# Optimization experiments

Measured on AMD Instinct MI355X. Metric: run time of the kernel, lower is better.

Reference implementation:

```python
import jax, jax.numpy as jnp
import numpy as np

B = 16384
A_SCALE = 1.7159
S_SCALE = 2.0 / 3.0
CONNECTIONS = [[0,1,2],[1,2,3],[2,3,4],[3,4,5],[0,4,5],[0,1,5],
               [0,1,2,3],[1,2,3,4],[2,3,4,5],[0,3,4,5],[0,1,4,5],[0,1,2,5],
               [0,1,3,4],[1,2,4,5],[0,2,3,5],[0,1,2,3,4,5]]

def _c3_mask():
    m = np.zeros((16, 6, 1, 1), dtype=np.float32)
    for i, conns in enumerate(CONNECTIONS):
        m[i, conns, 0, 0] = 1.0
    return jnp.asarray(m)

C3_MASK = _c3_mask()

def tanh_act(x):
    return A_SCALE * jnp.tanh(S_SCALE * x)

def conv_valid(x, w):
    # x: (B, Cin, H, W), w: (Cout, Cin, k, k) -> (B, Cout, H-k+1, W-k+1)
    return jax.lax.conv_general_dilated(
        x, w, window_strides=(1, 1), padding='VALID',
        dimension_numbers=('NCHW', 'OIHW', 'NCHW'))

def pool_affine(x, w, b):
    # Faithful to the torch 'efficient' path: reshape(B,C,H/2,W/2,2,2).mean((4,5)).
    # (This is a row-major regrouping, NOT true 2x2 block pooling.)
    bsz, c, h, wd = x.shape
    y = x.reshape(bsz, c, h // 2, wd // 2, 2, 2).mean(axis=(4, 5))
    return w.reshape(1, c, 1, 1) * y + b.reshape(1, c, 1, 1)


def setup_inputs() -> dict:
    key = jax.random.key(0)
    ks = jax.random.split(key, 14)
    inp = {
        'x':     jax.random.normal(ks[0], (B, 1, 32, 32), jnp.float32),
        'w1':    jax.random.normal(ks[1], (6, 1, 5, 5), jnp.float32) * 0.2,
        'b1':    jnp.zeros((6,), jnp.float32),
        's2_w':  jnp.ones((6,), jnp.float32),
        's2_b':  jnp.zeros((6,), jnp.float32),
        'w3':    jax.random.normal(ks[2], (16, 6, 5, 5), jnp.float32) * 0.1,
        'b3':    jnp.zeros((16,), jnp.float32),
        's4_w':  jnp.ones((16,), jnp.float32),
        's4_b':  jnp.zeros((16,), jnp.float32),
        'w5':    jax.random.normal(ks[3], (120, 16, 5, 5), jnp.float32) * 0.05,
        'b5':    jnp.zeros((120,), jnp.float32),
        'f6_w':  jax.random.normal(ks[4], (84, 120), jnp.float32) * 0.09,
        'f6_b':  jnp.zeros((84,), jnp.float32),
        'rbf_w': jax.random.bernoulli(ks[5], 0.3, (10, 84)).astype(jnp.float32),
    }
    return inp


def reference(x, w1, b1, s2_w, s2_b, w3, b3, s4_w, s4_b, w5, b5, f6_w, f6_b, rbf_w):
    # C1: full conv 1->6, per-filter scalar bias
    h = conv_valid(x, w1) + b1.reshape(1, -1, 1, 1)          # (B,6,28,28)
    h = tanh_act(h)
    # S2: avg pool (efficient reshape semantics) + learnable affine
    h = tanh_act(pool_affine(h, s2_w, s2_b))                  # (B,6,14,14)
    # C3: sparsely-connected conv 6->16, implemented as masked full conv
    h = conv_valid(h, w3 * C3_MASK) + b3.reshape(1, -1, 1, 1)  # (B,16,10,10)
    h = tanh_act(h)
    # S4
    h = tanh_act(pool_affine(h, s4_w, s4_b))                  # (B,16,5,5)
    # C5: full conv 16->120 on 5x5 -> 1x1, squeeze to (B,120)
    h = conv_valid(h, w5) + b5.reshape(1, -1, 1, 1)
    h = tanh_act(h.reshape(h.shape[0], 120))                  # (B,120)
    # F6
    h = tanh_act(h @ f6_w.T + f6_b)                           # (B,84)
    # RBF: squared euclidean distance to each class bitmap
    diff = h[:, None, :] - rbf_w[None, :, :]                  # (B,10,84)
    return jnp.sum(diff * diff, axis=2)                       # (B,10)
```

## Files before the change

### kernel.cpp

```cpp
#include <hip/hip_runtime.h>
#include <cstdint>


typedef unsigned int u32;

union U32H2 { u32 u; _Float16 h[2]; };
__device__ __forceinline__ float f16lo(u32 v) { U32H2 a; a.u = v; return (float)a.h[0]; }
__device__ __forceinline__ float f16hi(u32 v) { U32H2 a; a.u = v; return (float)a.h[1]; }
__device__ __forceinline__ u32 packh2(float a, float b) {
    U32H2 x; x.h[0] = (_Float16)a; x.h[1] = (_Float16)b; return x.u;
}

typedef _Float16 h2v __attribute__((ext_vector_type(2)));
union U32V2 { u32 u; h2v v; };

#if defined(__has_builtin)
#if __has_builtin(__builtin_amdgcn_fdot2)
#define HAVE_FDOT2 1
#endif
#endif

__device__ __forceinline__ float dot2(u32 a, u32 b, float c) {
    U32V2 x, y; x.u = a; y.u = b;
#ifdef HAVE_FDOT2
    return __builtin_amdgcn_fdot2(x.v, y.v, c, false);
#else
    return c + (float)x.v[0] * (float)y.v[0] + (float)x.v[1] * (float)y.v[1];
#endif
}

__device__ __forceinline__ u32 shf16(u32 lo, u32 hi) {
    return (lo >> 16) | (hi << 16);
}

__device__ __forceinline__ float tact(float v) {
    float e = __expf(1.3333333333f * v);
    return 1.7159f * (1.0f - 2.0f * __builtin_amdgcn_rcpf(e + 1.0f));
}

__device__ const int C3_NIC[16] = {3,3,3,3,3,3, 4,4,4,4,4,4,4,4,4, 6};
__device__ const int C3_ICL[96] = {
    0,1,2,0,0,0,  1,2,3,0,0,0,  2,3,4,0,0,0,  3,4,5,0,0,0,
    0,4,5,0,0,0,  0,1,5,0,0,0,  0,1,2,3,0,0,  1,2,3,4,0,0,
    2,3,4,5,0,0,  0,3,4,5,0,0,  0,1,4,5,0,0,  0,1,2,5,0,0,
    0,1,3,4,0,0,  1,2,4,5,0,0,  0,2,3,5,0,0,  0,1,2,3,4,5 };

#define WPK_W1 0
#define WPK_W3 96
#define WPK_W5 1536
#define WPK_F6 30336
#define WPK_N  35376

__global__ __launch_bounds__(256) void k_wpack(
    const float* __restrict__ w1, const float* __restrict__ w3,
    const float* __restrict__ w5, const float* __restrict__ f6w,
    u32* __restrict__ wpk)
{
    const int idx = blockIdx.x * 256 + threadIdx.x;
    if (idx >= WPK_N) return;
    float a = 0.0f, b = 0.0f;
    if (idx < 96) {
        if (idx < 90) {
            int ch = idx / 15, r = idx % 15, ky = r / 3, q = r % 3;
            a = w1[ch * 25 + ky * 5 + 2 * q];
            if (q < 2) b = w1[ch * 25 + ky * 5 + 2 * q + 1];
        }
    } else if (idx < WPK_W5) {
        int t = idx - WPK_W3;
        int p = t / 15, r = t % 15, ky = r / 3, q = r % 3;
        a = w3[p * 25 + ky * 5 + 2 * q];
        if (q < 2) b = w3[p * 25 + ky * 5 + 2 * q + 1];
    } else if (idx < WPK_F6) {
        int t = idx - WPK_W5;
        int c = t / 240, r = t % 240, g = r / 3, q = r % 3;
        a = w5[c * 400 + g * 5 + 2 * q];
        if (q < 2) b = w5[c * 400 + g * 5 + 2 * q + 1];
    } else {
        int t = idx - WPK_F6;
        int o = t / 60, i = t % 60;
        a = f6w[o * 120 + 2 * i];
        b = f6w[o * 120 + 2 * i + 1];
    }
    wpk[idx] = packh2(a, b);
}

__global__ __launch_bounds__(256) void k_tr(const float* __restrict__ x,
                                            u32* __restrict__ xp)
{
    __shared__ _Float16 lds[64 * 66];
    const int t = threadIdx.x;
    const int tb = blockIdx.x * 64;
    const int tp = blockIdx.y * 64;
    #pragma unroll
    for (int i = 0; i < 16; ++i) {
        int idx = i * 256 + t;
        int bl = idx >> 6, pl = idx & 63;
        lds[pl * 66 + bl] = (_Float16)x[(size_t)(tb + bl) * 1024 + tp + pl];
    }
    __syncthreads();
    #pragma unroll
    for (int j = 0; j < 8; ++j) {
        int idx = j * 256 + t;
        int pp = idx >> 6, bl = idx & 63;
        U32H2 u;
        u.h[0] = lds[(2 * pp) * 66 + bl];
        u.h[1] = lds[(2 * pp + 1) * 66 + bl];
        xp[(size_t)(blockIdx.y * 32 + pp) * 8192 + tb + bl] = u.u;
    }
}

__global__ __launch_bounds__(256) void k_c1s2(
    const u32* __restrict__ xp, const u32* __restrict__ wpk,
    const float* __restrict__ b1,
    const float* __restrict__ s2w, const float* __restrict__ s2b,
    u32* __restrict__ s2p, int ostr)
{
    const int sl = blockIdx.x * 256 + threadIdx.x;
    const int oy2 = blockIdx.y / 3;
    const int cp  = blockIdx.y % 3;
    const int y0 = 2 * oy2;
    const u32* xb = xp + sl;

    u32 wl[2][15];
    #pragma unroll
    for (int a = 0; a < 2; ++a)
        #pragma unroll
        for (int i = 0; i < 15; ++i) wl[a][i] = wpk[WPK_W1 + (2 * cp + a) * 15 + i];

    u32 cur[6][4];
    #pragma unroll
    for (int r = 0; r < 6; ++r)
        #pragma unroll
        for (int c = 0; c < 4; ++c)
            cur[r][c] = xb[(size_t)((y0 + r) * 16 + c) * 8192];

    float va[2][7], vb[2][7];

    #pragma unroll
    for (int qx = 0; qx < 7; ++qx) {
        float o[2][2][4];
        #pragma unroll
        for (int a = 0; a < 2; ++a) {
            const float bbv = b1[2 * cp + a];
            #pragma unroll
            for (int u = 0; u < 2; ++u)
                #pragma unroll
                for (int d = 0; d < 4; ++d) o[a][u][d] = bbv;
        }
        #pragma unroll
        for (int r = 0; r < 6; ++r) {
            const u32 s0 = shf16(cur[r][0], cur[r][1]);
            const u32 s1 = shf16(cur[r][1], cur[r][2]);
            const u32 s2 = shf16(cur[r][2], cur[r][3]);
            const u32 s3 = cur[r][3] >> 16;
            #pragma unroll
            for (int u = 0; u < 2; ++u) {
                const int ky = r - u;
                if (ky < 0 || ky > 4) continue;
                #pragma unroll
                for (int a = 0; a < 2; ++a) {
                    const u32 w0 = wl[a][ky * 3 + 0];
                    const u32 w1 = wl[a][ky * 3 + 1];
                    const u32 w2 = wl[a][ky * 3 + 2];
                    o[a][u][0] = dot2(cur[r][0], w0, dot2(cur[r][1], w1, dot2(cur[r][2], w2, o[a][u][0])));
                    o[a][u][1] = dot2(s0,        w0, dot2(s1,        w1, dot2(s2,        w2, o[a][u][1])));
                    o[a][u][2] = dot2(cur[r][1], w0, dot2(cur[r][2], w1, dot2(cur[r][3], w2, o[a][u][2])));
                    o[a][u][3] = dot2(s1,        w0, dot2(s2,        w1, dot2(s3,        w2, o[a][u][3])));
                }
            }
        }
        #pragma unroll
        for (int a = 0; a < 2; ++a) {
            const int ch = 2 * cp + a;
            const float sw = s2w[ch], sb = s2b[ch];
            float m0 = 0.25f * (tact(o[a][0][0]) + tact(o[a][0][1]) + tact(o[a][0][2]) + tact(o[a][0][3]));
            float m1 = 0.25f * (tact(o[a][1][0]) + tact(o[a][1][1]) + tact(o[a][1][2]) + tact(o[a][1][3]));
            va[a][qx] = tact(sw * m0 + sb);
            vb[a][qx] = tact(sw * m1 + sb);
        }
        if (qx < 6) {
            #pragma unroll
            for (int r = 0; r < 6; ++r) {
                cur[r][0] = cur[r][2];
                cur[r][1] = cur[r][3];
                cur[r][2] = xb[(size_t)((y0 + r) * 16 + 2 * qx + 4) * 8192];
                cur[r][3] = xb[(size_t)((y0 + r) * 16 + 2 * qx + 5) * 8192];
            }
        }
    }
    #pragma unroll
    for (int a = 0; a < 2; ++a) {
        u32 o7[7];
        o7[0] = packh2(va[a][0], va[a][1]);
        o7[1] = packh2(va[a][2], va[a][3]);
        o7[2] = packh2(va[a][4], va[a][5]);
        o7[3] = packh2(va[a][6], vb[a][0]);
        o7[4] = packh2(vb[a][1], vb[a][2]);
        o7[5] = packh2(vb[a][3], vb[a][4]);
        o7[6] = packh2(vb[a][5], vb[a][6]);
        const int ch = 2 * cp + a;
        const int f0 = ch * 98 + oy2 * 7;
        const int fh0 = f0 >> 1;
        uint2* p2 = (uint2*)s2p;
        uint2 t;
        if ((oy2 & 1) == 0) {
            t.x = o7[0]; t.y = o7[1]; p2[(size_t)(fh0 + 0) * ostr + sl] = t;
            t.x = o7[2]; t.y = o7[3]; p2[(size_t)(fh0 + 1) * ostr + sl] = t;
            t.x = o7[4]; t.y = o7[5]; p2[(size_t)(fh0 + 2) * ostr + sl] = t;
            s2p[((size_t)(fh0 + 3) * ostr + sl) * 2] = o7[6];
        } else {
            s2p[((size_t)fh0 * ostr + sl) * 2 + 1] = o7[0];
            t.x = o7[1]; t.y = o7[2]; p2[(size_t)(fh0 + 1) * ostr + sl] = t;
            t.x = o7[3]; t.y = o7[4]; p2[(size_t)(fh0 + 2) * ostr + sl] = t;
            t.x = o7[5]; t.y = o7[6]; p2[(size_t)(fh0 + 3) * ostr + sl] = t;
        }
    }
}

__global__ __launch_bounds__(256) void k_c3s4(
    const u32* __restrict__ s2p, const u32* __restrict__ wpk,
    const float* __restrict__ b3, const float* __restrict__ s4w,
    const float* __restrict__ s4b, u32* __restrict__ s4p, int nb)
{
    const int sl = blockIdx.x * 256 + threadIdx.x;
    const int oc = blockIdx.y / 5;
    const int y2 = blockIdx.y % 5;
    const int nic = C3_NIC[oc];
    const float bbv = b3[oc];

    float a2[2][10];
    #pragma unroll
    for (int u = 0; u < 2; ++u)
        #pragma unroll
        for (int ox = 0; ox < 10; ++ox) a2[u][ox] = bbv;

    for (int e = 0; e < nic; ++e) {
        const int ic = C3_ICL[oc * 6 + e];
        const uint2* sp2 = (const uint2*)s2p + (size_t)(ic * 49 + y2 * 7) * nb + sl;
        u32 wa[6][7];
        #pragma unroll
        for (int k = 0; k < 21; ++k) {
            const uint2 v = sp2[(size_t)k * nb];
            wa[(2 * k) / 7][(2 * k) % 7]         = v.x;
            wa[(2 * k + 1) / 7][(2 * k + 1) % 7] = v.y;
        }
        u32 wl[15];
        #pragma unroll
        for (int i = 0; i < 15; ++i) wl[i] = wpk[WPK_W3 + (oc * 6 + ic) * 15 + i];
        #pragma unroll
        for (int r = 0; r < 6; ++r) {
            u32 sh[7];
            #pragma unroll
            for (int j = 0; j < 6; ++j) sh[j] = shf16(wa[r][j], wa[r][j + 1]);
            sh[6] = wa[r][6] >> 16;
            #pragma unroll
            for (int u = 0; u < 2; ++u) {
                const int ky = r - u;
                if (ky < 0 || ky > 4) continue;
                const u32 w0 = wl[ky * 3 + 0];
                const u32 w1 = wl[ky * 3 + 1];
                const u32 w2 = wl[ky * 3 + 2];
                #pragma unroll
                for (int ox = 0; ox < 10; ox += 2) {
                    const int p = ox >> 1;
                    a2[u][ox]     = dot2(wa[r][p], w0, dot2(wa[r][p + 1], w1, dot2(wa[r][p + 2], w2, a2[u][ox])));
                    a2[u][ox + 1] = dot2(sh[p],    w0, dot2(sh[p + 1],    w1, dot2(sh[p + 2],    w2, a2[u][ox + 1])));
                }
            }
        }
    }
    float tv[20];
    #pragma unroll
    for (int u = 0; u < 2; ++u)
        #pragma unroll
        for (int ox = 0; ox < 10; ++ox) tv[u * 10 + ox] = tact(a2[u][ox]);
    const float swv = s4w[oc], sbv = s4b[oc];
    float so[5];
    #pragma unroll
    for (int x2 = 0; x2 < 5; ++x2)
        so[x2] = tact(0.25f * (tv[x2 * 4] + tv[x2 * 4 + 1] + tv[x2 * 4 + 2] + tv[x2 * 4 + 3]) * swv + sbv);
    const size_t g = (size_t)(oc * 5 + y2) * 3;
    s4p[(g + 0) * nb + sl] = packh2(so[0], so[1]);
    s4p[(g + 1) * nb + sl] = packh2(so[2], so[3]);
    s4p[(g + 2) * nb + sl] = packh2(so[4], 0.0f);
}

__global__ __launch_bounds__(256) void k_c5(
    const u32* __restrict__ s4p, const u32* __restrict__ wpk,
    const float* __restrict__ b5, u32* __restrict__ h5p, int nb)
{
    const int sl = blockIdx.x * 256 + threadIdx.x;
    const int chg = blockIdx.y;
    const u32* wp = wpk + WPK_W5 + chg * 10 * 240;
    float acc[10];
    #pragma unroll
    for (int c = 0; c < 10; ++c) acc[c] = b5[chg * 10 + c];
    #pragma unroll 4
    for (int i = 0; i < 240; ++i) {
        const u32 v = s4p[(size_t)i * nb + sl];
        #pragma unroll
        for (int c = 0; c < 10; ++c)
            acc[c] = dot2(v, wp[c * 240 + i], acc[c]);
    }
    #pragma unroll
    for (int j = 0; j < 5; ++j)
        h5p[(size_t)(chg * 5 + j) * nb + sl] =
            packh2(tact(acc[2 * j]), tact(acc[2 * j + 1]));
}

__global__ __launch_bounds__(256) void k_f6(
    const u32* __restrict__ h5p, const u32* __restrict__ wpk,
    const float* __restrict__ f6b, u32* __restrict__ h6p, int nb)
{
    const int sl = blockIdx.x * 256 + threadIdx.x;
    const int og = blockIdx.y;
    const u32* wp = wpk + WPK_F6 + og * 14 * 60;
    float acc[14];
    #pragma unroll
    for (int o = 0; o < 14; ++o) acc[o] = f6b[og * 14 + o];
    #pragma unroll 4
    for (int i = 0; i < 60; ++i) {
        const u32 v = h5p[(size_t)i * nb + sl];
        #pragma unroll
        for (int o = 0; o < 14; ++o)
            acc[o] = dot2(v, wp[o * 60 + i], acc[o]);
    }
    #pragma unroll
    for (int j = 0; j < 7; ++j)
        h6p[(size_t)(og * 7 + j) * nb + sl] =
            packh2(tact(acc[2 * j]), tact(acc[2 * j + 1]));
}

__global__ __launch_bounds__(256) void k_rbf(
    const u32* __restrict__ h6p, const float* __restrict__ rbf,
    float* __restrict__ out, int nb)
{
    const int sl = blockIdx.x * 256 + threadIdx.x;
    const int gy = blockIdx.y;
    float hv[84];
    #pragma unroll
    for (int i = 0; i < 42; ++i) {
        const u32 v = h6p[(size_t)i * nb + sl];
        hv[2 * i]     = f16lo(v);
        hv[2 * i + 1] = f16hi(v);
    }
    #pragma unroll
    for (int a = 0; a < 2; ++a) {
        const int c = 2 * gy + a;
        float acc = 0.0f;
        #pragma unroll 4
        for (int i = 0; i < 84; ++i) {
            float d = hv[i] - rbf[c * 84 + i];
            acc += d * d;
        }
        out[(size_t)sl * 10 + c] = acc;
    }
}

extern "C" void kernel_launch(void* const* d_in, const int* in_sizes, int n_in,
                              void* d_out, int out_size, void* d_ws, size_t ws_size,
                              hipStream_t stream)
{
    const float* x    = (const float*)d_in[0];
    const float* w1   = (const float*)d_in[1];
    const float* b1   = (const float*)d_in[2];
    const float* s2w  = (const float*)d_in[3];
    const float* s2b  = (const float*)d_in[4];
    const float* w3   = (const float*)d_in[5];
    const float* b3   = (const float*)d_in[6];
    const float* s4w  = (const float*)d_in[7];
    const float* s4b  = (const float*)d_in[8];
    const float* w5   = (const float*)d_in[9];
    const float* b5   = (const float*)d_in[10];
    const float* f6w  = (const float*)d_in[11];
    const float* f6b  = (const float*)d_in[12];
    const float* rbfw = (const float*)d_in[13];
    float* out = (float*)d_out;
    char* ws = (char*)d_ws;

    u32* WPK = (u32*)((char*)d_out +
                      (((size_t)out_size - (size_t)(WPK_N * 4)) & ~(size_t)7));
    k_wpack<<<dim3((WPK_N + 255) / 256), 256, 0, stream>>>(w1, w3, w5, f6w, WPK);

    if (ws_size >= 55312384) {
        u32* S2P = (u32*)(ws);
        u32* XP  = (u32*)(ws + 38535168);
        u32* S4P = (u32*)(ws + 38535168);
        u32* H5P = (u32*)(ws);
        u32* H6P = (u32*)(ws + 4194304);
        for (int c = 0; c < 2; ++c) {
            k_tr  <<<dim3(128, 16), 256, 0, stream>>>(x + (size_t)c * 8192 * 1024, XP);
            k_c1s2<<<dim3(32, 42), 256, 0, stream>>>(XP, WPK, b1, s2w, s2b,
                                                     S2P + (size_t)c * 16384, 16384);
        }
        k_c3s4<<<dim3(64, 80), 256, 0, stream>>>(S2P, WPK, b3, s4w, s4b, S4P, 16384);
        k_c5  <<<dim3(64, 12), 256, 0, stream>>>(S4P, WPK, b5, H5P, 16384);
        k_f6  <<<dim3(64, 6), 256, 0, stream>>>(H5P, WPK, f6b, H6P, 16384);
        k_rbf <<<dim3(64, 5), 256, 0, stream>>>(H6P, rbfw, out, 16384);
    } else {
        u32* XP  = (u32*)(ws);
        u32* S2P = (u32*)(ws + 16777216);
        u32* S4P = (u32*)(ws);
        u32* H5P = (u32*)(ws + 7864320);
        u32* H6P = (u32*)(ws + 9830400);
        for (int c = 0; c < 2; ++c) {
            k_tr  <<<dim3(128, 16), 256, 0, stream>>>(x + (size_t)c * 8192 * 1024, XP);
            k_c1s2<<<dim3(32, 42), 256, 0, stream>>>(XP, WPK, b1, s2w, s2b, S2P, 8192);
            k_c3s4<<<dim3(32, 80), 256, 0, stream>>>(S2P, WPK, b3, s4w, s4b, S4P, 8192);
            k_c5  <<<dim3(32, 12), 256, 0, stream>>>(S4P, WPK, b5, H5P, 8192);
            k_f6  <<<dim3(32, 6), 256, 0, stream>>>(H5P, WPK, f6b, H6P, 8192);
            k_rbf <<<dim3(32, 5), 256, 0, stream>>>(H6P, rbfw, out + (size_t)c * 8192 * 10, 8192);
        }
    }
}
```

Measured before the change: 333.7 us.

## Switch intermediate activations to per-sample contiguous layout with vectorized loads

```diff
diff --git a/kernel.cpp b/kernel.cpp
--- a/kernel.cpp
+++ b/kernel.cpp
@@ -85,41 +85,34 @@
 }
 
 __global__ __launch_bounds__(256) void k_tr(const float* __restrict__ x,
-                                            u32* __restrict__ xp)
-{
-    __shared__ _Float16 lds[64 * 66];
-    const int t = threadIdx.x;
-    const int tb = blockIdx.x * 64;
-    const int tp = blockIdx.y * 64;
-    #pragma unroll
-    for (int i = 0; i < 16; ++i) {
-        int idx = i * 256 + t;
-        int bl = idx >> 6, pl = idx & 63;
-        lds[pl * 66 + bl] = (_Float16)x[(size_t)(tb + bl) * 1024 + tp + pl];
-    }
-    __syncthreads();
-    #pragma unroll
-    for (int j = 0; j < 8; ++j) {
-        int idx = j * 256 + t;
-        int pp = idx >> 6, bl = idx & 63;
-        U32H2 u;
-        u.h[0] = lds[(2 * pp) * 66 + bl];
-        u.h[1] = lds[(2 * pp + 1) * 66 + bl];
-        xp[(size_t)(blockIdx.y * 32 + pp) * 8192 + tb + bl] = u.u;
+                                            u32* __restrict__ xpa)
+{
+    const int sl = blockIdx.x * 256 + threadIdx.x;
+    const int seg = blockIdx.y;
+    const float4* xb = (const float4*)(x + (size_t)sl * 1024 + seg * 128);
+    uint4* ob = (uint4*)(xpa + (size_t)sl * 512 + seg * 64);
+    #pragma unroll
+    for (int k = 0; k < 16; ++k) {
+        float4 a = xb[2 * k];
+        float4 b = xb[2 * k + 1];
+        uint4 o;
+        o.x = packh2(a.x, a.y); o.y = packh2(a.z, a.w);
+        o.z = packh2(b.x, b.y); o.w = packh2(b.z, b.w);
+        ob[k] = o;
     }
 }
 
 __global__ __launch_bounds__(256) void k_c1s2(
-    const u32* __restrict__ xp, const u32* __restrict__ wpk,
+    const u32* __restrict__ xpa, const u32* __restrict__ wpk,
     const float* __restrict__ b1,
     const float* __restrict__ s2w, const float* __restrict__ s2b,
-    u32* __restrict__ s2p, int ostr)
+    u32* __restrict__ s2pa)
 {
     const int sl = blockIdx.x * 256 + threadIdx.x;
     const int oy2 = blockIdx.y / 3;
     const int cp  = blockIdx.y % 3;
     const int y0 = 2 * oy2;
-    const u32* xb = xp + sl;
+    const u32* xb = xpa + (size_t)sl * 512 + y0 * 16;
 
     u32 wl[2][15];
     #pragma unroll
@@ -132,7 +125,7 @@
     for (int r = 0; r < 6; ++r)
         #pragma unroll
         for (int c = 0; c < 4; ++c)
-            cur[r][c] = xb[(size_t)((y0 + r) * 16 + c) * 8192];
+            cur[r][c] = xb[r * 16 + c];
 
     float va[2][7], vb[2][7];
 
@@ -183,8 +176,8 @@
             for (int r = 0; r < 6; ++r) {
                 cur[r][0] = cur[r][2];
                 cur[r][1] = cur[r][3];
-                cur[r][2] = xb[(size_t)((y0 + r) * 16 + 2 * qx + 4) * 8192];
-                cur[r][3] = xb[(size_t)((y0 + r) * 16 + 2 * qx + 5) * 8192];
+                cur[r][2] = xb[r * 16 + 2 * qx + 4];
+                cur[r][3] = xb[r * 16 + 2 * qx + 5];
             }
         }
     }
@@ -199,60 +192,48 @@
         o7[5] = packh2(vb[a][3], vb[a][4]);
         o7[6] = packh2(vb[a][5], vb[a][6]);
         const int ch = 2 * cp + a;
-        const int f0 = ch * 98 + oy2 * 7;
-        const int fh0 = f0 >> 1;
-        uint2* p2 = (uint2*)s2p;
-        uint2 t;
+        u32* op = s2pa + (size_t)sl * 588 + ch * 98 + oy2 * 7;
         if ((oy2 & 1) == 0) {
-            t.x = o7[0]; t.y = o7[1]; p2[(size_t)(fh0 + 0) * ostr + sl] = t;
-            t.x = o7[2]; t.y = o7[3]; p2[(size_t)(fh0 + 1) * ostr + sl] = t;
-            t.x = o7[4]; t.y = o7[5]; p2[(size_t)(fh0 + 2) * ostr + sl] = t;
-            s2p[((size_t)(fh0 + 3) * ostr + sl) * 2] = o7[6];
+            uint2 t;
+            t.x = o7[0]; t.y = o7[1]; *(uint2*)(op + 0) = t;
+            t.x = o7[2]; t.y = o7[3]; *(uint2*)(op + 2) = t;
+            t.x = o7[4]; t.y = o7[5]; *(uint2*)(op + 4) = t;
+            op[6] = o7[6];
         } else {
-            s2p[((size_t)fh0 * ostr + sl) * 2 + 1] = o7[0];
-            t.x = o7[1]; t.y = o7[2]; p2[(size_t)(fh0 + 1) * ostr + sl] = t;
-            t.x = o7[3]; t.y = o7[4]; p2[(size_t)(fh0 + 2) * ostr + sl] = t;
-            t.x = o7[5]; t.y = o7[6]; p2[(size_t)(fh0 + 3) * ostr + sl] = t;
-        }
-    }
-}
-
-__global__ __launch_bounds__(256) void k_c3s4(
-    const u32* __restrict__ s2p, const u32* __restrict__ wpk,
-    const float* __restrict__ b3, const float* __restrict__ s4w,
-    const float* __restrict__ s4b, u32* __restrict__ s4p, int nb)
-{
-    const int sl = blockIdx.x * 256 + threadIdx.x;
-    const int oc = blockIdx.y / 5;
-    const int y2 = blockIdx.y % 5;
-    const int nic = C3_NIC[oc];
-    const float bbv = b3[oc];
-
-    float a2[2][10];
-    #pragma unroll
-    for (int u = 0; u < 2; ++u)
-        #pragma unroll
-        for (int ox = 0; ox < 10; ++ox) a2[u][ox] = bbv;
-
-    for (int e = 0; e < nic; ++e) {
-        const int ic = C3_ICL[oc * 6 + e];
-        const uint2* sp2 = (const uint2*)s2p + (size_t)(ic * 49 + y2 * 7) * nb + sl;
-        u32 wa[6][7];
+            op[0] = o7[0];
+            uint2 t;
+            t.x = o7[1]; t.y = o7[2]; *(uint2*)(op + 1) = t;
+            t.x = o7[3]; t.y = o7[4]; *(uint2*)(op + 3) = t;
+            t.x = o7[5]; t.y = o7[6]; *(uint2*)(op + 5) = t;
+        }
+    }
+}
+
+template<int NIC>
+__device__ __forceinline__ void c3_body(
+    const u32* __restrict__ pb, const u32* __restrict__ wpk,
+    const int* __restrict__ icl, int oc, int y2, float a2[2][10])
+{
+    #pragma unroll
+    for (int e = 0; e < NIC; ++e) {
+        const int ic = icl[e];
+        const uint2* sp = (const uint2*)(pb + ic * 98 + 14 * y2);
+        u32 wf[42];
         #pragma unroll
         for (int k = 0; k < 21; ++k) {
-            const uint2 v = sp2[(size_t)k * nb];
-            wa[(2 * k) / 7][(2 * k) % 7]         = v.x;
-            wa[(2 * k + 1) / 7][(2 * k + 1) % 7] = v.y;
+            const uint2 v = sp[k];
+            wf[2 * k] = v.x; wf[2 * k + 1] = v.y;
         }
         u32 wl[15];
         #pragma unroll
         for (int i = 0; i < 15; ++i) wl[i] = wpk[WPK_W3 + (oc * 6 + ic) * 15 + i];
         #pragma unroll
         for (int r = 0; r < 6; ++r) {
+            const u32* wa = wf + 7 * r;
             u32 sh[7];
             #pragma unroll
-            for (int j = 0; j < 6; ++j) sh[j] = shf16(wa[r][j], wa[r][j + 1]);
-            sh[6] = wa[r][6] >> 16;
+            for (int j = 0; j < 6; ++j) sh[j] = shf16(wa[j], wa[j + 1]);
+            sh[6] = wa[6] >> 16;
             #pragma unroll
             for (int u = 0; u < 2; ++u) {
                 const int ky = r - u;
@@ -261,14 +242,39 @@
                 const u32 w1 = wl[ky * 3 + 1];
                 const u32 w2 = wl[ky * 3 + 2];
                 #pragma unroll
-                for (int ox = 0; ox < 10; ox += 2) {
-                    const int p = ox >> 1;
-                    a2[u][ox]     = dot2(wa[r][p], w0, dot2(wa[r][p + 1], w1, dot2(wa[r][p + 2], w2, a2[u][ox])));
-                    a2[u][ox + 1] = dot2(sh[p],    w0, dot2(sh[p + 1],    w1, dot2(sh[p + 2],    w2, a2[u][ox + 1])));
+                for (int p = 0; p < 5; ++p) {
+                    a2[u][2 * p]     = dot2(wa[p], w0, dot2(wa[p + 1], w1, dot2(wa[p + 2], w2, a2[u][2 * p])));
+                    a2[u][2 * p + 1] = dot2(sh[p], w0, dot2(sh[p + 1], w1, dot2(sh[p + 2], w2, a2[u][2 * p + 1])));
                 }
             }
         }
     }
+}
+
+__global__ __launch_bounds__(256) void k_c3s4(
+    const u32* __restrict__ s2pa, const u32* __restrict__ wpk,
+    const float* __restrict__ b3, const float* __restrict__ s4w,
+    const float* __restrict__ s4b, u32* __restrict__ s4pa)
+{
+    const int sl = blockIdx.x * 256 + threadIdx.x;
+    const int oc = blockIdx.y / 5;
+    const int y2 = blockIdx.y % 5;
+    const u32* pb = s2pa + (size_t)sl * 588;
+    const int* icl = &C3_ICL[oc * 6];
+    const float bbv = b3[oc];
+
+    float a2[2][10];
+    #pragma unroll
+    for (int u = 0; u < 2; ++u)
+        #pragma unroll
+        for (int ox = 0; ox < 10; ++ox) a2[u][ox] = bbv;
+
+    switch (C3_NIC[oc]) {
+        case 3:  c3_body<3>(pb, wpk, icl, oc, y2, a2); break;
+        case 4:  c3_body<4>(pb, wpk, icl, oc, y2, a2); break;
+        default: c3_body<6>(pb, wpk, icl, oc, y2, a2); break;
+    }
+
     float tv[20];
     #pragma unroll
     for (int u = 0; u < 2; ++u)
@@ -279,70 +285,81 @@
     #pragma unroll
     for (int x2 = 0; x2 < 5; ++x2)
         so[x2] = tact(0.25f * (tv[x2 * 4] + tv[x2 * 4 + 1] + tv[x2 * 4 + 2] + tv[x2 * 4 + 3]) * swv + sbv);
-    const size_t g = (size_t)(oc * 5 + y2) * 3;
-    s4p[(g + 0) * nb + sl] = packh2(so[0], so[1]);
-    s4p[(g + 1) * nb + sl] = packh2(so[2], so[3]);
-    s4p[(g + 2) * nb + sl] = packh2(so[4], 0.0f);
+    u32* op = s4pa + (size_t)sl * 240 + (oc * 5 + y2) * 3;
+    op[0] = packh2(so[0], so[1]);
+    op[1] = packh2(so[2], so[3]);
+    op[2] = packh2(so[4], 0.0f);
 }
 
 __global__ __launch_bounds__(256) void k_c5(
-    const u32* __restrict__ s4p, const u32* __restrict__ wpk,
-    const float* __restrict__ b5, u32* __restrict__ h5p, int nb)
+    const u32* __restrict__ s4pa, const u32* __restrict__ wpk,
+    const float* __restrict__ b5, u32* __restrict__ h5pa)
 {
     const int sl = blockIdx.x * 256 + threadIdx.x;
     const int chg = blockIdx.y;
-    const u32* wp = wpk + WPK_W5 + chg * 10 * 240;
+    const uint4* sb = (const uint4*)(s4pa + (size_t)sl * 240);
+    const u32* wb = wpk + WPK_W5 + chg * 2400;
     float acc[10];
     #pragma unroll
     for (int c = 0; c < 10; ++c) acc[c] = b5[chg * 10 + c];
     #pragma unroll 4
-    for (int i = 0; i < 240; ++i) {
-        const u32 v = s4p[(size_t)i * nb + sl];
-        #pragma unroll
-        for (int c = 0; c < 10; ++c)
-            acc[c] = dot2(v, wp[c * 240 + i], acc[c]);
-    }
+    for (int k = 0; k < 60; ++k) {
+        const uint4 v = sb[k];
+        #pragma unroll
+        for (int c = 0; c < 10; ++c) {
+            const u32* wp = wb + c * 240 + 4 * k;
+            acc[c] = dot2(v.w, wp[3], dot2(v.z, wp[2],
+                     dot2(v.y, wp[1], dot2(v.x, wp[0], acc[c]))));
+        }
+    }
+    u32* op = h5pa + (size_t)sl * 60 + chg * 5;
     #pragma unroll
     for (int j = 0; j < 5; ++j)
-        h5p[(size_t)(chg * 5 + j) * nb + sl] =
-            packh2(tact(acc[2 * j]), tact(acc[2 * j + 1]));
+        op[j] = packh2(tact(acc[2 * j]), tact(acc[2 * j + 1]));
 }
 
 __global__ __launch_bounds__(256) void k_f6(
-    const u32* __restrict__ h5p, const u32* __restrict__ wpk,
-    const float* __restrict__ f6b, u32* __restrict__ h6p, int nb)
+    const u32* __restrict__ h5pa, const u32* __restrict__ wpk,
+    const float* __restrict__ f6b, u32* __restrict__ h6pa)
 {
     const int sl = blockIdx.x * 256 + threadIdx.x;
     const int og = blockIdx.y;
-    const u32* wp = wpk + WPK_F6 + og * 14 * 60;
+    const uint4* hb = (const uint4*)(h5pa + (size_t)sl * 60);
+    const u32* wb = wpk + WPK_F6 + og * 14 * 60;
     float acc[14];
     #pragma unroll
     for (int o = 0; o < 14; ++o) acc[o] = f6b[og * 14 + o];
-    #pragma unroll 4
-    for (int i = 0; i < 60; ++i) {
-        const u32 v = h5p[(size_t)i * nb + sl];
-        #pragma unroll
-        for (int o = 0; o < 14; ++o)
-            acc[o] = dot2(v, wp[o * 60 + i], acc[o]);
-    }
+    #pragma unroll
+    for (int k = 0; k < 15; ++k) {
+        const uint4 v = hb[k];
+        #pragma unroll
+        for (int o = 0; o < 14; ++o) {
+            const u32* wp = wb + o * 60 + 4 * k;
+            acc[o] = dot2(v.w, wp[3], dot2(v.z, wp[2],
+                     dot2(v.y, wp[1], dot2(v.x, wp[0], acc[o]))));
+        }
+    }
+    u32* op = h6pa + (size_t)sl * 42 + og * 7;
     #pragma unroll
     for (int j = 0; j < 7; ++j)
-        h6p[(size_t)(og * 7 + j) * nb + sl] =
-            packh2(tact(acc[2 * j]), tact(acc[2 * j + 1]));
+        op[j] = packh2(tact(acc[2 * j]), tact(acc[2 * j + 1]));
 }
 
 __global__ __launch_bounds__(256) void k_rbf(
-    const u32* __restrict__ h6p, const float* __restrict__ rbf,
-    float* __restrict__ out, int nb)
+    const u32* __restrict__ h6pa, const float* __restrict__ rbf,
+    float* __restrict__ out)
 {
     const int sl = blockIdx.x * 256 + threadIdx.x;
     const int gy = blockIdx.y;
+    const uint2* hb = (const uint2*)(h6pa + (size_t)sl * 42);
     float hv[84];
     #pragma unroll
-    for (int i = 0; i < 42; ++i) {
-        const u32 v = h6p[(size_t)i * nb + sl];
-        hv[2 * i]     = f16lo(v);
-        hv[2 * i + 1] = f16hi(v);
+    for (int i = 0; i < 21; ++i) {
+        const uint2 v = hb[i];
+        hv[4 * i]     = f16lo(v.x);
+        hv[4 * i + 1] = f16hi(v.x);
+        hv[4 * i + 2] = f16lo(v.y);
+        hv[4 * i + 3] = f16hi(v.y);
     }
     #pragma unroll
     for (int a = 0; a < 2; ++a) {
@@ -389,14 +406,14 @@
         u32* H5P = (u32*)(ws);
         u32* H6P = (u32*)(ws + 4194304);
         for (int c = 0; c < 2; ++c) {
-            k_tr  <<<dim3(128, 16), 256, 0, stream>>>(x + (size_t)c * 8192 * 1024, XP);
+            k_tr  <<<dim3(32, 8), 256, 0, stream>>>(x + (size_t)c * 8192 * 1024, XP);
             k_c1s2<<<dim3(32, 42), 256, 0, stream>>>(XP, WPK, b1, s2w, s2b,
-                                                     S2P + (size_t)c * 16384, 16384);
-        }
-        k_c3s4<<<dim3(64, 80), 256, 0, stream>>>(S2P, WPK, b3, s4w, s4b, S4P, 16384);
-        k_c5  <<<dim3(64, 12), 256, 0, stream>>>(S4P, WPK, b5, H5P, 16384);
-        k_f6  <<<dim3(64, 6), 256, 0, stream>>>(H5P, WPK, f6b, H6P, 16384);
-        k_rbf <<<dim3(64, 5), 256, 0, stream>>>(H6P, rbfw, out, 16384);
+                                                     S2P + (size_t)c * 8192 * 588);
+        }
+        k_c3s4<<<dim3(64, 80), 256, 0, stream>>>(S2P, WPK, b3, s4w, s4b, S4P);
+        k_c5  <<<dim3(64, 12), 256, 0, stream>>>(S4P, WPK, b5, H5P);
+        k_f6  <<<dim3(64, 6), 256, 0, stream>>>(H5P, WPK, f6b, H6P);
+        k_rbf <<<dim3(64, 5), 256, 0, stream>>>(H6P, rbfw, out);
     } else {
         u32* XP  = (u32*)(ws);
         u32* S2P = (u32*)(ws + 16777216);
@@ -404,12 +421,12 @@
         u32* H5P = (u32*)(ws + 7864320);
         u32* H6P = (u32*)(ws + 9830400);
         for (int c = 0; c < 2; ++c) {
-            k_tr  <<<dim3(128, 16), 256, 0, stream>>>(x + (size_t)c * 8192 * 1024, XP);
-            k_c1s2<<<dim3(32, 42), 256, 0, stream>>>(XP, WPK, b1, s2w, s2b, S2P, 8192);
-            k_c3s4<<<dim3(32, 80), 256, 0, stream>>>(S2P, WPK, b3, s4w, s4b, S4P, 8192);
-            k_c5  <<<dim3(32, 12), 256, 0, stream>>>(S4P, WPK, b5, H5P, 8192);
-            k_f6  <<<dim3(32, 6), 256, 0, stream>>>(H5P, WPK, f6b, H6P, 8192);
-            k_rbf <<<dim3(32, 5), 256, 0, stream>>>(H6P, rbfw, out + (size_t)c * 8192 * 10, 8192);
-        }
-    }
-}
+            k_tr  <<<dim3(32, 8), 256, 0, stream>>>(x + (size_t)c * 8192 * 1024, XP);
+            k_c1s2<<<dim3(32, 42), 256, 0, stream>>>(XP, WPK, b1, s2w, s2b, S2P);
+            k_c3s4<<<dim3(32, 80), 256, 0, stream>>>(S2P, WPK, b3, s4w, s4b, S4P);
+            k_c5  <<<dim3(32, 12), 256, 0, stream>>>(S4P, WPK, b5, H5P);
+            k_f6  <<<dim3(32, 6), 256, 0, stream>>>(H5P, WPK, f6b, H6P);
+            k_rbf <<<dim3(32, 5), 256, 0, stream>>>(H6P, rbfw, out + (size_t)c * 8192 * 10);
+        }
+    }
+}
```

After: 425.5 us. 27.5% more time.

## Use pre-shifted half2 weights to drop odd-column shift ops in C1/C3

Applied to the files above, without the earlier changes.

```diff
diff --git a/kernel.cpp b/kernel.cpp
--- a/kernel.cpp
+++ b/kernel.cpp
@@ -29,10 +29,6 @@
 #endif
 }
 
-__device__ __forceinline__ u32 shf16(u32 lo, u32 hi) {
-    return (lo >> 16) | (hi << 16);
-}
-
 __device__ __forceinline__ float tact(float v) {
     float e = __expf(1.3333333333f * v);
     return 1.7159f * (1.0f - 2.0f * __builtin_amdgcn_rcpf(e + 1.0f));
@@ -45,11 +41,13 @@
     2,3,4,5,0,0,  0,3,4,5,0,0,  0,1,4,5,0,0,  0,1,2,5,0,0,
     0,1,3,4,0,0,  1,2,4,5,0,0,  0,2,3,5,0,0,  0,1,2,3,4,5 };
 
-#define WPK_W1 0
-#define WPK_W3 96
-#define WPK_W5 1536
-#define WPK_F6 30336
-#define WPK_N  35376
+#define WPK_W1  0
+#define WPK_W1S 96
+#define WPK_W3  192
+#define WPK_W3S 1632
+#define WPK_W5  3072
+#define WPK_F6  31872
+#define WPK_N   36912
 
 __global__ __launch_bounds__(256) void k_wpack(
     const float* __restrict__ w1, const float* __restrict__ w3,
@@ -59,17 +57,24 @@
     const int idx = blockIdx.x * 256 + threadIdx.x;
     if (idx >= WPK_N) return;
     float a = 0.0f, b = 0.0f;
-    if (idx < 96) {
-        if (idx < 90) {
-            int ch = idx / 15, r = idx % 15, ky = r / 3, q = r % 3;
-            a = w1[ch * 25 + ky * 5 + 2 * q];
-            if (q < 2) b = w1[ch * 25 + ky * 5 + 2 * q + 1];
+    if (idx < 192) {
+        const int s = idx >= 96;
+        const int t = idx - s * 96;
+        if (t < 90) {
+            int ch = t / 15, r = t % 15, ky = r / 3, q = r % 3;
+            const float* w = w1 + ch * 25 + ky * 5;
+            if (!s) { a = w[2 * q]; if (q < 2) b = w[2 * q + 1]; }
+            else if (q == 0) { b = w[0]; }
+            else { a = w[2 * q - 1]; b = w[2 * q]; }
         }
     } else if (idx < WPK_W5) {
-        int t = idx - WPK_W3;
+        const int s = (idx - WPK_W3) >= 1440;
+        const int t = idx - WPK_W3 - s * 1440;
         int p = t / 15, r = t % 15, ky = r / 3, q = r % 3;
-        a = w3[p * 25 + ky * 5 + 2 * q];
-        if (q < 2) b = w3[p * 25 + ky * 5 + 2 * q + 1];
+        const float* w = w3 + p * 25 + ky * 5;
+        if (!s) { a = w[2 * q]; if (q < 2) b = w[2 * q + 1]; }
+        else if (q == 0) { b = w[0]; }
+        else { a = w[2 * q - 1]; b = w[2 * q]; }
     } else if (idx < WPK_F6) {
         int t = idx - WPK_W5;
         int c = t / 240, r = t % 240, g = r / 3, q = r % 3;
@@ -121,11 +126,14 @@
     const int y0 = 2 * oy2;
     const u32* xb = xp + sl;
 
-    u32 wl[2][15];
-    #pragma unroll
-    for (int a = 0; a < 2; ++a)
-        #pragma unroll
-        for (int i = 0; i < 15; ++i) wl[a][i] = wpk[WPK_W1 + (2 * cp + a) * 15 + i];
+    u32 wl[2][15], wls[2][15];
+    #pragma unroll
+    for (int a = 0; a < 2; ++a) {
+        #pragma unroll
+        for (int i = 0; i < 15; ++i) wl[a][i]  = wpk[WPK_W1  + (2 * cp + a) * 15 + i];
+        #pragma unroll
+        for (int i = 0; i < 15; ++i) wls[a][i] = wpk[WPK_W1S + (2 * cp + a) * 15 + i];
+    }
 
     u32 cur[6][4];
     #pragma unroll
@@ -149,10 +157,6 @@
         }
         #pragma unroll
         for (int r = 0; r < 6; ++r) {
-            const u32 s0 = shf16(cur[r][0], cur[r][1]);
-            const u32 s1 = shf16(cur[r][1], cur[r][2]);
-            const u32 s2 = shf16(cur[r][2], cur[r][3]);
-            const u32 s3 = cur[r][3] >> 16;
             #pragma unroll
             for (int u = 0; u < 2; ++u) {
                 const int ky = r - u;
@@ -162,10 +166,13 @@
                     const u32 w0 = wl[a][ky * 3 + 0];
                     const u32 w1 = wl[a][ky * 3 + 1];
                     const u32 w2 = wl[a][ky * 3 + 2];
+                    const u32 v0 = wls[a][ky * 3 + 0];
+                    const u32 v1 = wls[a][ky * 3 + 1];
+                    const u32 v2 = wls[a][ky * 3 + 2];
                     o[a][u][0] = dot2(cur[r][0], w0, dot2(cur[r][1], w1, dot2(cur[r][2], w2, o[a][u][0])));
-                    o[a][u][1] = dot2(s0,        w0, dot2(s1,        w1, dot2(s2,        w2, o[a][u][1])));
+                    o[a][u][1] = dot2(cur[r][0], v0, dot2(cur[r][1], v1, dot2(cur[r][2], v2, o[a][u][1])));
                     o[a][u][2] = dot2(cur[r][1], w0, dot2(cur[r][2], w1, dot2(cur[r][3], w2, o[a][u][2])));
-                    o[a][u][3] = dot2(s1,        w0, dot2(s2,        w1, dot2(s3,        w2, o[a][u][3])));
+                    o[a][u][3] = dot2(cur[r][1], v0, dot2(cur[r][2], v1, dot2(cur[r][3], v2, o[a][u][3])));
                 }
             }
         }
@@ -217,42 +224,31 @@
     }
 }
 
-__global__ __launch_bounds__(256) void k_c3s4(
-    const u32* __restrict__ s2p, const u32* __restrict__ wpk,
-    const float* __restrict__ b3, const float* __restrict__ s4w,
-    const float* __restrict__ s4b, u32* __restrict__ s4p, int nb)
-{
-    const int sl = blockIdx.x * 256 + threadIdx.x;
-    const int oc = blockIdx.y / 5;
-    const int y2 = blockIdx.y % 5;
-    const int nic = C3_NIC[oc];
-    const float bbv = b3[oc];
-
-    float a2[2][10];
-    #pragma unroll
-    for (int u = 0; u < 2; ++u)
-        #pragma unroll
-        for (int ox = 0; ox < 10; ++ox) a2[u][ox] = bbv;
-
-    for (int e = 0; e < nic; ++e) {
-        const int ic = C3_ICL[oc * 6 + e];
-        const uint2* sp2 = (const uint2*)s2p + (size_t)(ic * 49 + y2 * 7) * nb + sl;
-        u32 wa[6][7];
+template<int NIC>
+__device__ __forceinline__ void c3_body(
+    const uint2* __restrict__ s2c, const u32* __restrict__ wpk,
+    const int* __restrict__ icl, int oc, int y2, int nb, int sl,
+    float a2[2][10])
+{
+    #pragma unroll
+    for (int e = 0; e < NIC; ++e) {
+        const int ic = icl[e];
+        const uint2* sp = s2c + (size_t)(ic * 49 + y2 * 7) * nb + sl;
+        u32 wa_[6][7];
         #pragma unroll
         for (int k = 0; k < 21; ++k) {
-            const uint2 v = sp2[(size_t)k * nb];
-            wa[(2 * k) / 7][(2 * k) % 7]         = v.x;
-            wa[(2 * k + 1) / 7][(2 * k + 1) % 7] = v.y;
-        }
-        u32 wl[15];
-        #pragma unroll
-        for (int i = 0; i < 15; ++i) wl[i] = wpk[WPK_W3 + (oc * 6 + ic) * 15 + i];
+            const uint2 v = sp[(size_t)k * nb];
+            wa_[(2 * k) / 7][(2 * k) % 7]         = v.x;
+            wa_[(2 * k + 1) / 7][(2 * k + 1) % 7] = v.y;
+        }
+        u32 wl[15], wls[15];
+        #pragma unroll
+        for (int i = 0; i < 15; ++i) wl[i]  = wpk[WPK_W3  + (oc * 6 + ic) * 15 + i];
+        #pragma unroll
+        for (int i = 0; i < 15; ++i) wls[i] = wpk[WPK_W3S + (oc * 6 + ic) * 15 + i];
         #pragma unroll
         for (int r = 0; r < 6; ++r) {
-            u32 sh[7];
-            #pragma unroll
-            for (int j = 0; j < 6; ++j) sh[j] = shf16(wa[r][j], wa[r][j + 1]);
-            sh[6] = wa[r][6] >> 16;
+            const u32* wa = wa_[r];
             #pragma unroll
             for (int u = 0; u < 2; ++u) {
                 const int ky = r - u;
@@ -260,15 +256,43 @@
                 const u32 w0 = wl[ky * 3 + 0];
                 const u32 w1 = wl[ky * 3 + 1];
                 const u32 w2 = wl[ky * 3 + 2];
+                const u32 v0 = wls[ky * 3 + 0];
+                const u32 v1 = wls[ky * 3 + 1];
+                const u32 v2 = wls[ky * 3 + 2];
                 #pragma unroll
-                for (int ox = 0; ox < 10; ox += 2) {
-                    const int p = ox >> 1;
-                    a2[u][ox]     = dot2(wa[r][p], w0, dot2(wa[r][p + 1], w1, dot2(wa[r][p + 2], w2, a2[u][ox])));
-                    a2[u][ox + 1] = dot2(sh[p],    w0, dot2(sh[p + 1],    w1, dot2(sh[p + 2],    w2, a2[u][ox + 1])));
+                for (int p = 0; p < 5; ++p) {
+                    a2[u][2 * p]     = dot2(wa[p], w0, dot2(wa[p + 1], w1, dot2(wa[p + 2], w2, a2[u][2 * p])));
+                    a2[u][2 * p + 1] = dot2(wa[p], v0, dot2(wa[p + 1], v1, dot2(wa[p + 2], v2, a2[u][2 * p + 1])));
                 }
             }
         }
     }
+}
+
+__global__ __launch_bounds__(256) void k_c3s4(
+    const u32* __restrict__ s2p, const u32* __restrict__ wpk,
+    const float* __restrict__ b3, const float* __restrict__ s4w,
+    const float* __restrict__ s4b, u32* __restrict__ s4p, int nb)
+{
+    const int sl = blockIdx.x * 256 + threadIdx.x;
+    const int oc = blockIdx.y / 5;
+    const int y2 = blockIdx.y % 5;
+    const uint2* s2c = (const uint2*)s2p;
+    const int* icl = &C3_ICL[oc * 6];
+    const float bbv = b3[oc];
+
+    float a2[2][10];
+    #pragma unroll
+    for (int u = 0; u < 2; ++u)
+        #pragma unroll
+        for (int ox = 0; ox < 10; ++ox) a2[u][ox] = bbv;
+
+    switch (C3_NIC[oc]) {
+        case 3:  c3_body<3>(s2c, wpk, icl, oc, y2, nb, sl, a2); break;
+        case 4:  c3_body<4>(s2c, wpk, icl, oc, y2, nb, sl, a2); break;
+        default: c3_body<6>(s2c, wpk, icl, oc, y2, nb, sl, a2); break;
+    }
+
     float tv[20];
     #pragma unroll
     for (int u = 0; u < 2; ++u)
```

Result: faster. 321.5 us (-3.6%).
